# Kernel optimization log

Measured on AMD Instinct MI355X. Metric: run time of the kernel, lower is better.

The kernel has to match this reference:

```python
import jax, jax.numpy as jnp
import numpy as np

B, N, H, HEADS = 8, 1024, 512, 4  # batch graphs, nodes/graph, graph_hsz, attention heads
R = 64  # relations per graph (passthrough)


def setup_inputs() -> dict:
    key = jax.random.key(0)
    k1, k2, k3, k4, k5, k6, k7 = jax.random.split(key, 7)
    adjs = jax.random.randint(k1, (B, N, N), 0, 2, dtype=jnp.int32)  # 0 => masked
    nodes = jax.random.normal(k2, (B, N, H), dtype=jnp.float32)
    triples = jax.random.normal(k3, (B, R, H), dtype=jnp.float32)   # unused in gat path
    relations = jax.random.normal(k4, (B, R, H), dtype=jnp.float32)  # passthrough
    node_num = jnp.full((B,), N, dtype=jnp.int32)  # all graphs full => no padding branch
    s = 1.0 / np.sqrt(H)
    Wq = (jax.random.normal(k5, (H, H), dtype=jnp.float32) * s)
    Wk = (jax.random.normal(k6, (H, H), dtype=jnp.float32) * s)
    Wv = (jax.random.normal(k7, (H, H), dtype=jnp.float32) * s)
    return {"adjs": adjs, "triples": triples, "nodes": nodes, "node_num": node_num,
            "relations": relations, "Wq": Wq, "Wk": Wk, "Wv": Wv}


def reference(adjs, triples, nodes, node_num, relations, Wq, Wk, Wv):
    b, n, h = nodes.shape
    dk = h // HEADS
    scale = 1.0 / jnp.sqrt(jnp.float32(h))  # torch divides by sqrt(key_dim)=sqrt(H)

    def to_heads(x, W):  # [B,N,H] -> [B,heads,N,dk]; matches split(dim=-1)+stack
        return (x @ W).reshape(b, n, HEADS, dk).transpose(0, 2, 1, 3)

    Q = to_heads(nodes, Wq)
    K = to_heads(nodes, Wk)
    V = to_heads(nodes, Wv)
    att = jnp.einsum('bhnd,bhmd->bhnm', Q, K) * scale
    att = jnp.where((adjs == 0)[:, None, :, :], -jnp.inf, att)
    p = jax.nn.softmax(att, axis=-1)  # dropout_p = blockdrop = 0.0 => identity
    out = jnp.einsum('bhnm,bhmd->bhnd', p, V)
    out = out.transpose(0, 2, 1, 3).reshape(b, n, h)  # concat heads along feature dim
    out = jax.nn.relu(out)
    return (out, relations)
```

## Files before the change

kernel.cpp:

```cpp
#include <hip/hip_runtime.h>
#include <stdint.h>

typedef __attribute__((ext_vector_type(4))) float f32x4;
typedef __attribute__((ext_vector_type(8))) short bf16x8;
typedef unsigned long long ull;

#define GLB_AS const __attribute__((address_space(1)))
#define LDS_AS __attribute__((address_space(3)))

__device__ __forceinline__ short f2bf(float f) {
    union { float f; unsigned u; } x; x.f = f;
    unsigned r = x.u + 0x7FFFu + ((x.u >> 16) & 1u);
    return (short)(r >> 16);
}

__global__ void k_cvt_nodes(const float* __restrict__ in, short* __restrict__ out, int n) {
    int i = (blockIdx.x * 256 + threadIdx.x) * 8;
    if (i + 8 > n) return;
    float4 a = *(const float4*)(in + i);
    float4 b = *(const float4*)(in + i + 4);
    bf16x8 v;
    v[0] = f2bf(a.x); v[1] = f2bf(a.y); v[2] = f2bf(a.z); v[3] = f2bf(a.w);
    v[4] = f2bf(b.x); v[5] = f2bf(b.y); v[6] = f2bf(b.z); v[7] = f2bf(b.w);
    *(bf16x8*)(out + i) = v;
}

__global__ void k_cvt_wT(const float* __restrict__ Wq, const float* __restrict__ Wk,
                         const float* __restrict__ Wv, short* __restrict__ WT) {
    int g = blockIdx.x * 256 + threadIdx.x;
    int j = g >> 9;
    int k = g & 511;
    int w = j >> 9;
    int n = j & 511;
    const float* W = (w == 0) ? Wq : (w == 1) ? Wk : Wv;
    WT[g] = f2bf(W[k * 512 + n]);
}

__global__ void k_pack_adj(const int* __restrict__ adjs, unsigned* __restrict__ packed) {
    int g = blockIdx.x * 256 + threadIdx.x;
    int wv = g >> 6, lane = g & 63;
    ull m = __ballot(adjs[(size_t)wv * 64 + lane] != 0);
    if (lane == 0) *(ull*)(packed + (size_t)wv * 2) = m;
}

__global__ __launch_bounds__(256) void k_gemm_qkv(const short* __restrict__ A,
                                                  const short* __restrict__ WT,
                                                  short* __restrict__ C) {
    __shared__ short Asm[2][128 * 32];
    __shared__ short Bsm[2][128 * 32];
    const int tid = threadIdx.x;
    const int l = tid & 63, w = tid >> 6;
    const int wr = w >> 1, wc = w & 1;
    const int c16 = l & 15, g = l >> 4;
    const int row0 = blockIdx.x * 128, n0 = blockIdx.y * 128;
    f32x4 acc[4][4] = {};

    auto stage = [&](int kt, int bsel) {
        const int k0 = kt * 32;
#pragma unroll
        for (int i = 0; i < 2; ++i) {
            int ch = tid + 256 * i;
            int r = ch >> 2, gc = ch & 3;
            __builtin_amdgcn_global_load_lds((GLB_AS unsigned*)(A + (row0 + r) * 512 + k0 + 8 * gc),
                                             (LDS_AS unsigned*)(&Asm[bsel][ch * 8]), 16, 0, 0);
            __builtin_amdgcn_global_load_lds((GLB_AS unsigned*)(WT + (n0 + r) * 512 + k0 + 8 * gc),
                                             (LDS_AS unsigned*)(&Bsm[bsel][ch * 8]), 16, 0, 0);
        }
    };

    stage(0, 0);
    asm volatile("s_waitcnt vmcnt(0)" ::: "memory");
    __syncthreads();

    for (int kt = 0; kt < 16; ++kt) {
        const int cur = kt & 1;
        if (kt < 15) stage(kt + 1, cur ^ 1);
        bf16x8 af[4], bfr[4];
#pragma unroll
        for (int mf = 0; mf < 4; ++mf)
            af[mf] = *(const bf16x8*)&Asm[cur][(wr * 64 + mf * 16 + c16) * 32 + 8 * g];
#pragma unroll
        for (int nf = 0; nf < 4; ++nf)
            bfr[nf] = *(const bf16x8*)&Bsm[cur][(wc * 64 + nf * 16 + c16) * 32 + 8 * g];
#pragma unroll
        for (int mf = 0; mf < 4; ++mf)
#pragma unroll
            for (int nf = 0; nf < 4; ++nf)
                acc[mf][nf] = __builtin_amdgcn_mfma_f32_16x16x32_bf16(af[mf], bfr[nf], acc[mf][nf], 0, 0, 0);
        asm volatile("s_waitcnt vmcnt(0)" ::: "memory");
        __syncthreads();
    }
#pragma unroll
    for (int mf = 0; mf < 4; ++mf)
#pragma unroll
        for (int nf = 0; nf < 4; ++nf)
#pragma unroll
            for (int r = 0; r < 4; ++r) {
                int row = row0 + wr * 64 + mf * 16 + 4 * g + r;
                int col = n0 + wc * 64 + nf * 16 + c16;
                C[row * 1536 + col] = f2bf(acc[mf][nf][r]);
            }
}

__global__ __launch_bounds__(256) void k_transpose_v(const short* __restrict__ QKV, short* __restrict__ Vt) {
    __shared__ short tile[64 * 65];
    const int b = blockIdx.x, n0 = blockIdx.y * 64, d0 = blockIdx.z * 64;
    const int t = threadIdx.x;
#pragma unroll
    for (int i = 0; i < 16; ++i) {
        int idx = t + 256 * i;
        int nn = idx >> 6, dd = idx & 63;
        tile[nn * 65 + dd] = QKV[(b * 1024 + n0 + nn) * 1536 + 1024 + d0 + dd];
    }
    __syncthreads();
#pragma unroll
    for (int i = 0; i < 16; ++i) {
        int idx = t + 256 * i;
        int dd = idx >> 6, nn = idx & 63;
        Vt[(b * 512 + d0 + dd) * 1024 + n0 + nn] = tile[nn * 65 + dd];
    }
}

__global__ __launch_bounds__(512) void k_attn(const short* __restrict__ QKV, const short* __restrict__ Vt,
                                              const unsigned* __restrict__ packed, float* __restrict__ out) {
    __shared__ short Ksm[2][64 * 128];
    __shared__ short Vsm[2][128 * 64];
    __shared__ short Psm[128 * 72];
    const int bh = blockIdx.x;
    const int b = bh >> 2, h = bh & 3;
    const int q0 = blockIdx.y * 128;
    const int tid = threadIdx.x, l = tid & 63, wid = tid >> 6;
    const int c16 = l & 15, g = l >> 4;
    const int qw = q0 + wid * 16;
    const float scale = 0.044194173824159216f;

    bf16x8 aq[4];
    const short* Qrow = QKV + (size_t)(b * 1024 + qw + c16) * 1536 + h * 128;
#pragma unroll
    for (int kf = 0; kf < 4; ++kf)
        aq[kf] = *(const bf16x8*)(Qrow + kf * 32 + 8 * g);

    f32x4 acc_o[8] = {};
    float l_lane[4] = {0.f, 0.f, 0.f, 0.f};

    const short* Kbase = QKV + (size_t)(b * 1024) * 1536 + 512 + h * 128;
    const short* Vtbase = Vt + (size_t)(b * 512 + h * 128) * 1024;
    const ull* adjp = (const ull*)packed + (size_t)(b * 1024 + qw + 4 * g) * 16;

    auto stage = [&](int t, int bsel) {
        const int m0 = t * 64;
#pragma unroll
        for (int i = 0; i < 2; ++i) {
            int ch = tid + 512 * i;
            int mr = ch >> 4, gc = ch & 15;
            int gs = gc ^ (mr & 7);
            __builtin_amdgcn_global_load_lds((GLB_AS unsigned*)(Kbase + (size_t)(m0 + mr) * 1536 + 8 * gs),
                                             (LDS_AS unsigned*)(&Ksm[bsel][ch * 8]), 16, 0, 0);
        }
#pragma unroll
        for (int i = 0; i < 2; ++i) {
            int ch = tid + 512 * i;
            int dr = ch >> 3, gc = ch & 7;
            int gs = gc ^ (dr & 7);
            __builtin_amdgcn_global_load_lds((GLB_AS unsigned*)(Vtbase + (size_t)dr * 1024 + m0 + 8 * gs),
                                             (LDS_AS unsigned*)(&Vsm[bsel][ch * 8]), 16, 0, 0);
        }
    };

    ull mcur[4], mnxt[4] = {0, 0, 0, 0};
#pragma unroll
    for (int r = 0; r < 4; ++r) mcur[r] = adjp[r * 16];
    stage(0, 0);
    asm volatile("s_waitcnt vmcnt(0)" ::: "memory");
    __syncthreads();

    for (int t = 0; t < 16; ++t) {
        const int cur = t & 1;
        if (t < 15) {
#pragma unroll
            for (int r = 0; r < 4; ++r) mnxt[r] = adjp[r * 16 + t + 1];
            stage(t + 1, cur ^ 1);
        }

        f32x4 s[4] = {};
        __builtin_amdgcn_s_setprio(1);
#pragma unroll
        for (int nf = 0; nf < 4; ++nf) {
            const int mrow = nf * 16 + c16;
#pragma unroll
            for (int kf = 0; kf < 4; ++kf) {
                int chunk = (kf * 4 + g) ^ (mrow & 7);
                bf16x8 bk = *(const bf16x8*)&Ksm[cur][mrow * 128 + chunk * 8];
                s[nf] = __builtin_amdgcn_mfma_f32_16x16x32_bf16(aq[kf], bk, s[nf], 0, 0, 0);
            }
        }
        __builtin_amdgcn_s_setprio(0);

#pragma unroll
        for (int r = 0; r < 4; ++r) {
            unsigned mlo = (unsigned)mcur[r];
            unsigned mhi = (unsigned)(mcur[r] >> 32);
#pragma unroll
            for (int nf = 0; nf < 4; ++nf) {
                unsigned hw = (nf < 2) ? mlo : mhi;
                unsigned bit = (hw >> ((nf & 1) * 16 + c16)) & 1u;
                float e = __expf(s[nf][r] * scale);
                float pv = bit ? e : 0.f;
                l_lane[r] += pv;
                Psm[(wid * 16 + 4 * g + r) * 72 + nf * 16 + c16] = f2bf(pv);
            }
        }

        asm volatile("s_waitcnt vmcnt(8)" ::: "memory");
        __builtin_amdgcn_s_barrier();

        __builtin_amdgcn_s_setprio(1);
#pragma unroll
        for (int ks = 0; ks < 2; ++ks) {
            bf16x8 ap = *(const bf16x8*)&Psm[(wid * 16 + c16) * 72 + ks * 32 + 8 * g];
#pragma unroll
            for (int df = 0; df < 8; ++df) {
                const int drow = df * 16 + c16;
                int chunk = (ks * 4 + g) ^ (drow & 7);
                bf16x8 bv = *(const bf16x8*)&Vsm[cur][drow * 64 + chunk * 8];
                acc_o[df] = __builtin_amdgcn_mfma_f32_16x16x32_bf16(ap, bv, acc_o[df], 0, 0, 0);
            }
        }
        __builtin_amdgcn_s_setprio(0);

#pragma unroll
        for (int r = 0; r < 4; ++r) mcur[r] = mnxt[r];

        asm volatile("s_waitcnt vmcnt(2)" ::: "memory");
        __builtin_amdgcn_s_barrier();
    }

    float inv_l[4];
#pragma unroll
    for (int r = 0; r < 4; ++r) {
        float ls = l_lane[r];
        ls += __shfl_xor(ls, 1);
        ls += __shfl_xor(ls, 2);
        ls += __shfl_xor(ls, 4);
        ls += __shfl_xor(ls, 8);
        inv_l[r] = 1.f / ls;
    }
#pragma unroll
    for (int df = 0; df < 8; ++df)
#pragma unroll
        for (int r = 0; r < 4; ++r) {
            int q = qw + 4 * g + r;
            float o = fmaxf(acc_o[df][r] * inv_l[r], 0.f);
            out[(size_t)(b * 1024 + q) * 512 + h * 128 + df * 16 + c16] = o;
        }
}

__global__ void k_copy_rel(const float* __restrict__ in, float* __restrict__ out, int n) {
    int i = (blockIdx.x * 256 + threadIdx.x) * 4;
    if (i + 4 > n) return;
    *(float4*)(out + i) = *(const float4*)(in + i);
}

extern "C" void kernel_launch(void* const* d_in, const int* in_sizes, int n_in,
                              void* d_out, int out_size, void* d_ws, size_t ws_size,
                              hipStream_t stream) {
    const int*   adjs      = (const int*)d_in[0];
    const float* nodes     = (const float*)d_in[2];
    const float* relations = (const float*)d_in[4];
    const float* Wq        = (const float*)d_in[5];
    const float* Wk        = (const float*)d_in[6];
    const float* Wv        = (const float*)d_in[7];

    char* ws = (char*)d_ws;
    short* nodes_bf   = (short*)(ws);
    short* WT         = (short*)(ws + 8388608);
    short* QKV        = (short*)(ws + 9961472);
    short* Vt         = (short*)(ws + 35127296);
    unsigned* adjpack = (unsigned*)(ws + 43515904);

    float* out     = (float*)d_out;
    float* out_rel = out + 4194304;

    k_cvt_nodes<<<dim3(2048), dim3(256), 0, stream>>>(nodes, nodes_bf, 4194304);
    k_cvt_wT<<<dim3(3072), dim3(256), 0, stream>>>(Wq, Wk, Wv, WT);
    k_pack_adj<<<dim3(32768), dim3(256), 0, stream>>>(adjs, adjpack);
    k_gemm_qkv<<<dim3(64, 12), dim3(256), 0, stream>>>(nodes_bf, WT, QKV);
    k_transpose_v<<<dim3(8, 16, 8), dim3(256), 0, stream>>>(QKV, Vt);
    k_attn<<<dim3(32, 8), dim3(512), 0, stream>>>(QKV, Vt, adjpack, out);
    k_copy_rel<<<dim3(256), dim3(256), 0, stream>>>(relations, out_rel, 262144);
}
```

Before: 91.28 us.

## Split attention over key halves with combine kernel, register-direct V loads

The attention kernel is split along the key dimension into two halves (blockIdx.z), which doubles the grid to 512 blocks of 256 threads. Each wave now covers 32 query rows, and V fragments are loaded straight from global memory into registers instead of being staged through LDS. Partial outputs (fp32 into out, bf16 into the workspace) and row sums are merged by a new combine kernel that applies normalization and ReLU. The QKV GEMM also gets a swizzled 1D block order for cache locality, and exp is switched to exp2 with a prescaled constant. In exchange it adds an extra kernel pass, extra partial-output traffic, and bf16 rounding of the second half's partial sum.

```diff
diff --git a/kernel.cpp b/kernel.cpp
--- a/kernel.cpp
+++ b/kernel.cpp
@@ -12,6 +12,10 @@
     union { float f; unsigned u; } x; x.f = f;
     unsigned r = x.u + 0x7FFFu + ((x.u >> 16) & 1u);
     return (short)(r >> 16);
+}
+__device__ __forceinline__ float bf2f(short s) {
+    union { unsigned u; float f; } x; x.u = ((unsigned)(unsigned short)s) << 16;
+    return x.f;
 }
 
 __global__ void k_cvt_nodes(const float* __restrict__ in, short* __restrict__ out, int n) {
@@ -52,7 +56,9 @@
     const int l = tid & 63, w = tid >> 6;
     const int wr = w >> 1, wc = w & 1;
     const int c16 = l & 15, g = l >> 4;
-    const int row0 = blockIdx.x * 128, n0 = blockIdx.y * 128;
+    const int wg = blockIdx.x;
+    const int swz = (wg & 7) * 96 + (wg >> 3);
+    const int row0 = (swz / 12) * 128, n0 = (swz % 12) * 128;
     f32x4 acc[4][4] = {};
 
     auto stage = [&](int kt, int bsel) {
@@ -121,68 +127,63 @@
     }
 }
 
-__global__ __launch_bounds__(512) void k_attn(const short* __restrict__ QKV, const short* __restrict__ Vt,
-                                              const unsigned* __restrict__ packed, float* __restrict__ out) {
+__global__ __launch_bounds__(256, 2) void k_attn(const short* __restrict__ QKV, const short* __restrict__ Vt,
+                                                 const unsigned* __restrict__ packed,
+                                                 float* __restrict__ o0, short* __restrict__ o1,
+                                                 float* __restrict__ lpart) {
     __shared__ short Ksm[2][64 * 128];
-    __shared__ short Vsm[2][128 * 64];
-    __shared__ short Psm[128 * 72];
+    __shared__ short Psm[128 * 68];
     const int bh = blockIdx.x;
     const int b = bh >> 2, h = bh & 3;
     const int q0 = blockIdx.y * 128;
+    const int mh = blockIdx.z;
     const int tid = threadIdx.x, l = tid & 63, wid = tid >> 6;
     const int c16 = l & 15, g = l >> 4;
-    const int qw = q0 + wid * 16;
-    const float scale = 0.044194173824159216f;
-
-    bf16x8 aq[4];
-    const short* Qrow = QKV + (size_t)(b * 1024 + qw + c16) * 1536 + h * 128;
-#pragma unroll
-    for (int kf = 0; kf < 4; ++kf)
-        aq[kf] = *(const bf16x8*)(Qrow + kf * 32 + 8 * g);
-
-    f32x4 acc_o[8] = {};
-    float l_lane[4] = {0.f, 0.f, 0.f, 0.f};
+    const int qw = q0 + wid * 32;
+    const float kscale = 0.06375872022286384f;
+    const int mbase = mh * 512;
+
+    bf16x8 aq[2][4];
+#pragma unroll
+    for (int qb = 0; qb < 2; ++qb)
+#pragma unroll
+        for (int kf = 0; kf < 4; ++kf)
+            aq[qb][kf] = *(const bf16x8*)(QKV + (size_t)(b * 1024 + qw + qb * 16 + c16) * 1536 + h * 128 + kf * 32 + 8 * g);
+
+    f32x4 acc[2][8] = {};
+    float l_lane[2][4] = {};
 
     const short* Kbase = QKV + (size_t)(b * 1024) * 1536 + 512 + h * 128;
-    const short* Vtbase = Vt + (size_t)(b * 512 + h * 128) * 1024;
+    const short* Vtb = Vt + (size_t)(b * 512 + h * 128) * 1024;
     const ull* adjp = (const ull*)packed + (size_t)(b * 1024 + qw + 4 * g) * 16;
 
-    auto stage = [&](int t, int bsel) {
-        const int m0 = t * 64;
-#pragma unroll
-        for (int i = 0; i < 2; ++i) {
-            int ch = tid + 512 * i;
+    auto stageK = [&](int t, int bsel) {
+        const int m0 = mbase + t * 64;
+#pragma unroll
+        for (int i = 0; i < 4; ++i) {
+            int ch = tid + 256 * i;
             int mr = ch >> 4, gc = ch & 15;
             int gs = gc ^ (mr & 7);
             __builtin_amdgcn_global_load_lds((GLB_AS unsigned*)(Kbase + (size_t)(m0 + mr) * 1536 + 8 * gs),
                                              (LDS_AS unsigned*)(&Ksm[bsel][ch * 8]), 16, 0, 0);
         }
-#pragma unroll
-        for (int i = 0; i < 2; ++i) {
-            int ch = tid + 512 * i;
-            int dr = ch >> 3, gc = ch & 7;
-            int gs = gc ^ (dr & 7);
-            __builtin_amdgcn_global_load_lds((GLB_AS unsigned*)(Vtbase + (size_t)dr * 1024 + m0 + 8 * gs),
-                                             (LDS_AS unsigned*)(&Vsm[bsel][ch * 8]), 16, 0, 0);
-        }
     };
 
-    ull mcur[4], mnxt[4] = {0, 0, 0, 0};
-#pragma unroll
-    for (int r = 0; r < 4; ++r) mcur[r] = adjp[r * 16];
-    stage(0, 0);
+    ull mcur[2][4], mnxt[2][4] = {};
+#pragma unroll
+    for (int qb = 0; qb < 2; ++qb)
+#pragma unroll
+        for (int r = 0; r < 4; ++r) mcur[qb][r] = adjp[(qb * 16 + r) * 16 + mh * 8];
+    stageK(0, 0);
     asm volatile("s_waitcnt vmcnt(0)" ::: "memory");
-    __syncthreads();
-
-    for (int t = 0; t < 16; ++t) {
+    __builtin_amdgcn_s_barrier();
+
+    for (int t = 0; t < 8; ++t) {
         const int cur = t & 1;
-        if (t < 15) {
-#pragma unroll
-            for (int r = 0; r < 4; ++r) mnxt[r] = adjp[r * 16 + t + 1];
-            stage(t + 1, cur ^ 1);
-        }
-
-        f32x4 s[4] = {};
+        const int m0 = mbase + t * 64;
+        if (t < 7) stageK(t + 1, cur ^ 1);
+
+        f32x4 s[2][4] = {};
         __builtin_amdgcn_s_setprio(1);
 #pragma unroll
         for (int nf = 0; nf < 4; ++nf) {
@@ -191,68 +192,137 @@
             for (int kf = 0; kf < 4; ++kf) {
                 int chunk = (kf * 4 + g) ^ (mrow & 7);
                 bf16x8 bk = *(const bf16x8*)&Ksm[cur][mrow * 128 + chunk * 8];
-                s[nf] = __builtin_amdgcn_mfma_f32_16x16x32_bf16(aq[kf], bk, s[nf], 0, 0, 0);
+                s[0][nf] = __builtin_amdgcn_mfma_f32_16x16x32_bf16(aq[0][kf], bk, s[0][nf], 0, 0, 0);
+                s[1][nf] = __builtin_amdgcn_mfma_f32_16x16x32_bf16(aq[1][kf], bk, s[1][nf], 0, 0, 0);
             }
         }
         __builtin_amdgcn_s_setprio(0);
 
+        bf16x8 bv0[8];
+#pragma unroll
+        for (int df = 0; df < 8; ++df)
+            bv0[df] = *(const bf16x8*)(Vtb + (size_t)(df * 16 + c16) * 1024 + m0 + 8 * g);
+        if (t < 7) {
+#pragma unroll
+            for (int qb = 0; qb < 2; ++qb)
+#pragma unroll
+                for (int r = 0; r < 4; ++r) mnxt[qb][r] = adjp[(qb * 16 + r) * 16 + mh * 8 + t + 1];
+        }
+
+#pragma unroll
+        for (int qb = 0; qb < 2; ++qb)
+#pragma unroll
+            for (int r = 0; r < 4; ++r) {
+                unsigned mlo = (unsigned)mcur[qb][r];
+                unsigned mhi = (unsigned)(mcur[qb][r] >> 32);
+#pragma unroll
+                for (int nf = 0; nf < 4; ++nf) {
+                    unsigned hw = (nf < 2) ? mlo : mhi;
+                    unsigned bit = (hw >> ((nf & 1) * 16 + c16)) & 1u;
+                    float e = __builtin_amdgcn_exp2f(s[qb][nf][r] * kscale);
+                    float pv = bit ? e : 0.f;
+                    l_lane[qb][r] += pv;
+                    Psm[(wid * 32 + qb * 16 + 4 * g + r) * 68 + nf * 16 + c16] = f2bf(pv);
+                }
+            }
+
+        __builtin_amdgcn_s_setprio(1);
+#pragma unroll
+        for (int qb = 0; qb < 2; ++qb) {
+            bf16x8 ap = *(const bf16x8*)&Psm[(wid * 32 + qb * 16 + c16) * 68 + 8 * g];
+#pragma unroll
+            for (int df = 0; df < 8; ++df)
+                acc[qb][df] = __builtin_amdgcn_mfma_f32_16x16x32_bf16(ap, bv0[df], acc[qb][df], 0, 0, 0);
+        }
+        __builtin_amdgcn_s_setprio(0);
+        bf16x8 bv1[8];
+#pragma unroll
+        for (int df = 0; df < 8; ++df)
+            bv1[df] = *(const bf16x8*)(Vtb + (size_t)(df * 16 + c16) * 1024 + m0 + 32 + 8 * g);
+        __builtin_amdgcn_s_setprio(1);
+#pragma unroll
+        for (int qb = 0; qb < 2; ++qb) {
+            bf16x8 ap = *(const bf16x8*)&Psm[(wid * 32 + qb * 16 + c16) * 68 + 32 + 8 * g];
+#pragma unroll
+            for (int df = 0; df < 8; ++df)
+                acc[qb][df] = __builtin_amdgcn_mfma_f32_16x16x32_bf16(ap, bv1[df], acc[qb][df], 0, 0, 0);
+        }
+        __builtin_amdgcn_s_setprio(0);
+
+#pragma unroll
+        for (int qb = 0; qb < 2; ++qb)
+#pragma unroll
+            for (int r = 0; r < 4; ++r) mcur[qb][r] = mnxt[qb][r];
+
+        asm volatile("s_waitcnt vmcnt(0)" ::: "memory");
+        __builtin_amdgcn_s_barrier();
+    }
+
+    float lred[2][4];
+#pragma unroll
+    for (int qb = 0; qb < 2; ++qb)
 #pragma unroll
         for (int r = 0; r < 4; ++r) {
-            unsigned mlo = (unsigned)mcur[r];
-            unsigned mhi = (unsigned)(mcur[r] >> 32);
-#pragma unroll
-            for (int nf = 0; nf < 4; ++nf) {
-                unsigned hw = (nf < 2) ? mlo : mhi;
-                unsigned bit = (hw >> ((nf & 1) * 16 + c16)) & 1u;
-                float e = __expf(s[nf][r] * scale);
-                float pv = bit ? e : 0.f;
-                l_lane[r] += pv;
-                Psm[(wid * 16 + 4 * g + r) * 72 + nf * 16 + c16] = f2bf(pv);
-            }
-        }
-
-        asm volatile("s_waitcnt vmcnt(8)" ::: "memory");
-        __builtin_amdgcn_s_barrier();
-
-        __builtin_amdgcn_s_setprio(1);
-#pragma unroll
-        for (int ks = 0; ks < 2; ++ks) {
-            bf16x8 ap = *(const bf16x8*)&Psm[(wid * 16 + c16) * 72 + ks * 32 + 8 * g];
-#pragma unroll
-            for (int df = 0; df < 8; ++df) {
-                const int drow = df * 16 + c16;
-                int chunk = (ks * 4 + g) ^ (drow & 7);
-                bf16x8 bv = *(const bf16x8*)&Vsm[cur][drow * 64 + chunk * 8];
-                acc_o[df] = __builtin_amdgcn_mfma_f32_16x16x32_bf16(ap, bv, acc_o[df], 0, 0, 0);
-            }
-        }
-        __builtin_amdgcn_s_setprio(0);
-
-#pragma unroll
-        for (int r = 0; r < 4; ++r) mcur[r] = mnxt[r];
-
-        asm volatile("s_waitcnt vmcnt(2)" ::: "memory");
-        __builtin_amdgcn_s_barrier();
-    }
-
-    float inv_l[4];
-#pragma unroll
-    for (int r = 0; r < 4; ++r) {
-        float ls = l_lane[r];
-        ls += __shfl_xor(ls, 1);
-        ls += __shfl_xor(ls, 2);
-        ls += __shfl_xor(ls, 4);
-        ls += __shfl_xor(ls, 8);
-        inv_l[r] = 1.f / ls;
-    }
-#pragma unroll
-    for (int df = 0; df < 8; ++df)
-#pragma unroll
-        for (int r = 0; r < 4; ++r) {
-            int q = qw + 4 * g + r;
-            float o = fmaxf(acc_o[df][r] * inv_l[r], 0.f);
-            out[(size_t)(b * 1024 + q) * 512 + h * 128 + df * 16 + c16] = o;
-        }
+            float ls = l_lane[qb][r];
+            ls += __shfl_xor(ls, 1);
+            ls += __shfl_xor(ls, 2);
+            ls += __shfl_xor(ls, 4);
+            ls += __shfl_xor(ls, 8);
+            lred[qb][r] = ls;
+        }
+
+    if (mh == 0) {
+#pragma unroll
+        for (int qb = 0; qb < 2; ++qb)
+#pragma unroll
+            for (int df = 0; df < 8; ++df)
+#pragma unroll
+                for (int r = 0; r < 4; ++r) {
+                    int q = qw + qb * 16 + 4 * g + r;
+                    o0[(size_t)(b * 1024 + q) * 512 + h * 128 + df * 16 + c16] = acc[qb][df][r];
+                }
+    } else {
+#pragma unroll
+        for (int qb = 0; qb < 2; ++qb)
+#pragma unroll
+            for (int df = 0; df < 8; ++df)
+#pragma unroll
+                for (int r = 0; r < 4; ++r) {
+                    int q = qw + qb * 16 + 4 * g + r;
+                    o1[(size_t)(b * 1024 + q) * 512 + h * 128 + df * 16 + c16] = f2bf(acc[qb][df][r]);
+                }
+    }
+    if (c16 == 0) {
+#pragma unroll
+        for (int qb = 0; qb < 2; ++qb)
+#pragma unroll
+            for (int r = 0; r < 4; ++r)
+                lpart[mh * 32768 + (b * 4 + h) * 1024 + qw + qb * 16 + 4 * g + r] = lred[qb][r];
+    }
+}
+
+__global__ void k_combine(float* __restrict__ out, const short* __restrict__ o1,
+                          const float* __restrict__ lp) {
+    int i = (blockIdx.x * 256 + threadIdx.x) * 8;
+    int b = i >> 19;
+    int q = (i >> 9) & 1023;
+    int h = (i >> 7) & 3;
+    int lidx = (b * 4 + h) * 1024 + q;
+    float inv = 1.f / (lp[lidx] + lp[32768 + lidx]);
+    float4 a0 = *(const float4*)(out + i);
+    float4 a1 = *(const float4*)(out + i + 4);
+    bf16x8 c = *(const bf16x8*)(o1 + i);
+    float4 r0, r1;
+    r0.x = fmaxf((a0.x + bf2f(c[0])) * inv, 0.f);
+    r0.y = fmaxf((a0.y + bf2f(c[1])) * inv, 0.f);
+    r0.z = fmaxf((a0.z + bf2f(c[2])) * inv, 0.f);
+    r0.w = fmaxf((a0.w + bf2f(c[3])) * inv, 0.f);
+    r1.x = fmaxf((a1.x + bf2f(c[4])) * inv, 0.f);
+    r1.y = fmaxf((a1.y + bf2f(c[5])) * inv, 0.f);
+    r1.z = fmaxf((a1.z + bf2f(c[6])) * inv, 0.f);
+    r1.w = fmaxf((a1.w + bf2f(c[7])) * inv, 0.f);
+    *(float4*)(out + i) = r0;
+    *(float4*)(out + i + 4) = r1;
 }
 
 __global__ void k_copy_rel(const float* __restrict__ in, float* __restrict__ out, int n) {
@@ -277,6 +347,8 @@
     short* QKV        = (short*)(ws + 9961472);
     short* Vt         = (short*)(ws + 35127296);
     unsigned* adjpack = (unsigned*)(ws + 43515904);
+    short* opart1 = (short*)(ws);
+    float* lpart  = (float*)(ws + 8388608);
 
     float* out     = (float*)d_out;
     float* out_rel = out + 4194304;
@@ -284,8 +356,9 @@
     k_cvt_nodes<<<dim3(2048), dim3(256), 0, stream>>>(nodes, nodes_bf, 4194304);
     k_cvt_wT<<<dim3(3072), dim3(256), 0, stream>>>(Wq, Wk, Wv, WT);
     k_pack_adj<<<dim3(32768), dim3(256), 0, stream>>>(adjs, adjpack);
-    k_gemm_qkv<<<dim3(64, 12), dim3(256), 0, stream>>>(nodes_bf, WT, QKV);
+    k_gemm_qkv<<<dim3(768), dim3(256), 0, stream>>>(nodes_bf, WT, QKV);
     k_transpose_v<<<dim3(8, 16, 8), dim3(256), 0, stream>>>(QKV, Vt);
-    k_attn<<<dim3(32, 8), dim3(512), 0, stream>>>(QKV, Vt, adjpack, out);
+    k_attn<<<dim3(32, 8, 2), dim3(256), 0, stream>>>(QKV, Vt, adjpack, out, opart1, lpart);
+    k_combine<<<dim3(2048), dim3(256), 0, stream>>>(out, opart1, lpart);
     k_copy_rel<<<dim3(256), dim3(256), 0, stream>>>(relations, out_rel, 262144);
 }
```

Result: slower. 107.8 us (+18.1%).
